# Performance work log

Measured on AMD Instinct MI355X. Metric: run time of the kernel, lower is better.

The kernel has to match this reference:

```python
import jax, jax.numpy as jnp
from jax import lax
import numpy as np

N = 262144    # input_size (mesh nodes)
B = 16        # batch of snapshots
LAT = 16      # dims_latent
HID = 512     # intermediate fc width
NFC = 16      # num_final_channels
START = 4097  # inv_conv_start
SPLIT = NFC * START
SFC = 2       # number of space-filling curves
K, S, P = 32, 4, 16             # kernel/stride/padding (dimension==2)
OPS = (1, 1, 0)                 # output_paddings of decoder convT chain
CH = ((16, 8), (8, 4), (4, 1))  # (in,out) channels per decoder convT layer


def conv_t(x, w, b, op):
    # torch ConvTranspose1d: w [Cin,Cout,K], stride=S, padding=P, output_padding=op
    # equivalent to lhs-dilated cross-correlation with flipped, transposed kernel
    rhs = jnp.flip(w, -1).transpose(1, 0, 2)  # [Cout,Cin,K]
    y = lax.conv_general_dilated(x, rhs, (1,), [(K - 1 - P, K - 1 - P + op)],
                                 lhs_dilation=(S,),
                                 dimension_numbers=('NCH', 'OIH', 'NCH'))
    return y + b[None, :, None]


def setup_inputs() -> dict:
    key = jax.random.key(0)
    ks = jax.random.split(key, 32)
    inp = {}
    inp['x'] = jax.random.normal(ks[0], (B, LAT), jnp.float32)
    inp['fc1_w'] = jax.random.normal(ks[1], (LAT, HID), jnp.float32) * 0.1
    inp['fc1_b'] = jnp.zeros((HID,), jnp.float32)
    inp['fc2_w'] = jax.random.normal(ks[2], (HID, SFC * SPLIT), jnp.float32) * 0.02
    inp['fc2_b'] = jnp.zeros((SFC * SPLIT,), jnp.float32)
    idx = 3
    for i in range(SFC):
        for j, (ci, co) in enumerate(CH):
            inp[f'ct{i}{j}_w'] = jax.random.normal(ks[idx], (ci, co, K), jnp.float32) * 0.05
            inp[f'ct{i}{j}_b'] = jnp.zeros((co,), jnp.float32)
            idx += 1
        # NearestNeighbouring(size=N, initial_weight=1/3, num_neigh=3)
        inp[f'sp{i}_w'] = jnp.full((N, 3), 1.0 / 3.0, jnp.float32)
        inp[f'sp{i}_b'] = jnp.zeros((N,), jnp.float32)
        oi = jax.random.permutation(ks[idx], N).astype(jnp.int32)
        idx += 1
        inp[f'ord{i}'] = oi
        inp[f'minus{i}'] = jnp.concatenate([oi[:1], oi[:-1]])  # find_minus_neigh
        inp[f'plus{i}'] = jnp.concatenate([oi[1:], oi[-1:]])   # find_plus_neigh
    # final_sp: NearestNeighbouring(size=N, initial_weight=1/sfc_nums, num_neigh=sfc_nums)
    inp['fsp_w'] = jnp.full((N, SFC), 1.0 / SFC, jnp.float32)
    inp['fsp_b'] = jnp.zeros((N,), jnp.float32)
    return inp


def reference(x, fc1_w, fc1_b, fc2_w, fc2_b,
              ct00_w, ct00_b, ct01_w, ct01_b, ct02_w, ct02_b,
              ct10_w, ct10_b, ct11_w, ct11_b, ct12_w, ct12_b,
              sp0_w, sp0_b, sp1_w, sp1_b, fsp_w, fsp_b,
              ord0, minus0, plus0, ord1, minus1, plus1):
    act = jnp.tanh  # unstructured default activation
    h = act(x @ fc1_w + fc1_b)
    h = act(h @ fc2_w + fc2_b)          # [B, SFC*SPLIT]
    h = h.reshape(-1, SPLIT, SFC)
    cts = (((ct00_w, ct00_b), (ct01_w, ct01_b), (ct02_w, ct02_b)),
           ((ct10_w, ct10_b), (ct11_w, ct11_b), (ct12_w, ct12_b)))
    sps = ((sp0_w, sp0_b), (sp1_w, sp1_b))
    ords = ((minus0, ord0, plus0), (minus1, ord1, plus1))
    zs = []
    for i in range(SFC):
        b = h[..., i].reshape(-1, NFC, START)   # [B,16,4097]
        for j in range(len(CH)):
            w, bb = cts[i][j]
            b = act(conv_t(b, w, bb, OPS[j]))
        b = b.reshape(-1, N)                    # [B, N]
        m, o, p = ords[i]
        # SFC gather of (minus, self, plus) neighbors -> [B, N, 3]
        tt = jnp.stack([b[:, m], b[:, o], b[:, p]], axis=-1)
        w, bb = sps[i]
        zs.append(act(jnp.sum(tt * w, -1) + bb))
    # combine the SFC branches with the final learned weighted sum
    z = act(jnp.sum(jnp.stack(zs, -1) * fsp_w, -1) + fsp_b)  # [B, N]
    return z
```

## Files before the change

### kernel.cpp

```cpp
#include <hip/hip_runtime.h>
#include <hip/hip_bf16.h>

#define BATCH 16
#define LAT 16
#define HID 512
#define NFC 16
#define START_ 4097
#define NSFC 2
#define NMESH 262144
#define JTOT 131104
#define HB_BR_STRIDE 1048832

#define L1 16385
#define L1S 16388
#define L2 65537
#define L2S 65540
#define L3 262144

#define Y1_SZ (BATCH*8*L1S)
#define Y2_SZ (BATCH*4*L2S)
#define Y3_SZ (BATCH*L3)

__global__ __launch_bounds__(256) void k_fc1(const float* __restrict__ x,
                                             const float* __restrict__ w,
                                             const float* __restrict__ bias,
                                             float* __restrict__ h1) {
    int j = blockIdx.x * 256 + threadIdx.x;
    float acc[BATCH];
    float bv = bias[j];
#pragma unroll
    for (int b = 0; b < BATCH; ++b) acc[b] = bv;
#pragma unroll
    for (int k = 0; k < LAT; ++k) {
        float wv = w[k * HID + j];
#pragma unroll
        for (int b = 0; b < BATCH; ++b)
            acc[b] = fmaf(x[b * LAT + k], wv, acc[b]);
    }
#pragma unroll
    for (int b = 0; b < BATCH; ++b) h1[b * HID + j] = tanhf(acc[b]);
}

__global__ __launch_bounds__(256) void k_fc2(const float* __restrict__ h1,
                                             const float* __restrict__ w,
                                             const float* __restrict__ bias,
                                             float* __restrict__ hb) {
    int j = blockIdx.x * 256 + threadIdx.x;
    if (j >= JTOT) return;
    float acc[BATCH];
    float bv = bias[j];
#pragma unroll
    for (int b = 0; b < BATCH; ++b) acc[b] = bv;
#pragma unroll 8
    for (int k = 0; k < HID; ++k) {
        float wv = w[(size_t)k * JTOT + j];
#pragma unroll
        for (int b = 0; b < BATCH; ++b)
            acc[b] = fmaf(h1[b * HID + k], wv, acc[b]);
    }
    int i = j & 1;
    int s = j >> 1;
    int c = s / START_;
    int t = s - c * START_;
    float* hp = hb + (size_t)i * HB_BR_STRIDE + c * START_ + t;
#pragma unroll
    for (int b = 0; b < BATCH; ++b)
        hp[(size_t)b * (NFC * START_)] = tanhf(acc[b]);
}

template <int CIN, int COUT, int WCO, int WT>
__global__ __launch_bounds__(256) void k_conv(const float* __restrict__ xb,
                                              float* __restrict__ yb,
                                              const float* __restrict__ w0g,
                                              const float* __restrict__ w1g,
                                              const float* __restrict__ b0g,
                                              const float* __restrict__ b1g,
                                              int LIN, int LINS, int LOUT, int LOUTS,
                                              int xbs, int ybs) {
    constexpr int SROW = WT * 256 + 12;
    constexpr int SROW4 = SROW / 4;
    __shared__ __align__(16) float sx[CIN * SROW];

    const int br = blockIdx.z;
    const float* x = xb + (size_t)br * xbs;
    float* y = yb + (size_t)br * ybs;
    const float* wg = br ? w1g : w0g;
    const float* bg = br ? b1g : b0g;
    const int b = blockIdx.y;
    const int t0 = blockIdx.x * (WT * 1024);
    const int q0 = (t0 + 16) >> 2;

    for (int idx = threadIdx.x; idx < CIN * SROW; idx += 256) {
        int ci = idx / SROW;
        int sr = idx - ci * SROW;
        int s = q0 - 8 + sr;
        sx[idx] = (s >= 0 && s < LIN) ? x[(size_t)(b * CIN + ci) * LINS + s] : 0.f;
    }
    __syncthreads();

    const int wv = __builtin_amdgcn_readfirstlane((int)(threadIdx.x >> 6));
    const int lane = threadIdx.x & 63;
    constexpr int WAVES_CO = 4 / WT;
    const int wt = wv / WAVES_CO;
    const int co0 = (wv % WAVES_CO) * WCO;

    float acc[WCO][16];
#pragma unroll
    for (int cw = 0; cw < WCO; ++cw) {
        float bv = bg[co0 + cw];
#pragma unroll
        for (int e = 0; e < 16; ++e) acc[cw][e] = bv;
    }

    const int qrel4 = wt * 64 + lane;
    const float4* sx4 = (const float4*)sx;
#pragma unroll 1
    for (int ci = 0; ci < CIN; ++ci) {
        float4 A = sx4[ci * SROW4 + qrel4];
        float4 Bv = sx4[ci * SROW4 + qrel4 + 1];
        float4 Cv = sx4[ci * SROW4 + qrel4 + 2];
        float xv[12] = {A.x, A.y, A.z, A.w, Bv.x, Bv.y, Bv.z, Bv.w,
                        Cv.x, Cv.y, Cv.z, Cv.w};
        const float* wp = wg + (ci * COUT + co0) * 32;
#pragma unroll
        for (int cw = 0; cw < WCO; ++cw) {
            const float* wpc = wp + cw * 32;
#pragma unroll
            for (int d = 0; d < 8; ++d)
#pragma unroll
                for (int m = 0; m < 4; ++m)
#pragma unroll
                    for (int j = 0; j < 4; ++j)
                        acc[cw][m * 4 + j] =
                            fmaf(xv[m + 8 - d], wpc[4 * d + j], acc[cw][m * 4 + j]);
        }
    }

    const int t_lane = t0 + wt * 1024 + lane * 16;
#pragma unroll
    for (int cw = 0; cw < WCO; ++cw) {
        float* yp = y + (size_t)(b * COUT + co0 + cw) * LOUTS + t_lane;
        if (t_lane + 15 < LOUT) {
#pragma unroll
            for (int c4 = 0; c4 < 4; ++c4) {
                float4 o;
                o.x = tanhf(acc[cw][c4 * 4 + 0]);
                o.y = tanhf(acc[cw][c4 * 4 + 1]);
                o.z = tanhf(acc[cw][c4 * 4 + 2]);
                o.w = tanhf(acc[cw][c4 * 4 + 3]);
                ((float4*)yp)[c4] = o;
            }
        } else {
            for (int e = 0; e < 16; ++e)
                if (t_lane + e < LOUT) yp[e] = tanhf(acc[cw][e]);
        }
    }
}

__global__ __launch_bounds__(256) void k_final(const float* __restrict__ y30,
                                               const float* __restrict__ y31,
                                               const int* __restrict__ ord0,
                                               const int* __restrict__ ord1,
                                               const float* __restrict__ sw0,
                                               const float* __restrict__ sb0,
                                               const float* __restrict__ sw1,
                                               const float* __restrict__ sb1,
                                               const float* __restrict__ fw,
                                               const float* __restrict__ fb,
                                               float* __restrict__ out) {
    __shared__ int i0[258], i1[258];
    __shared__ float c0[258], c1[258];
    const int tid = threadIdx.x;
    const int n0 = blockIdx.x * 256;
    const int n = n0 + tid;

    for (int jj = tid; jj < 258; jj += 256) {
        int nn = n0 - 1 + jj;
        nn = nn < 0 ? 0 : (nn > NMESH - 1 ? NMESH - 1 : nn);
        i0[jj] = ord0[nn];
        i1[jj] = ord1[nn];
    }

    const float w00 = sw0[n * 3], w01 = sw0[n * 3 + 1], w02 = sw0[n * 3 + 2];
    const float w10 = sw1[n * 3], w11 = sw1[n * 3 + 1], w12 = sw1[n * 3 + 2];
    const float s0b = sb0[n], s1b = sb1[n];
    const float f0 = fw[n * 2], f1 = fw[n * 2 + 1], fbv = fb[n];

    for (int b = 0; b < BATCH; ++b) {
        __syncthreads();
        for (int jj = tid; jj < 258; jj += 256) {
            c0[jj] = y30[b * NMESH + i0[jj]];
            c1[jj] = y31[b * NMESH + i1[jj]];
        }
        __syncthreads();
        float z0 = tanhf(w00 * c0[tid] + w01 * c0[tid + 1] + w02 * c0[tid + 2] + s0b);
        float z1 = tanhf(w10 * c1[tid] + w11 * c1[tid + 1] + w12 * c1[tid + 2] + s1b);
        out[b * NMESH + n] = tanhf(f0 * z0 + f1 * z1 + fbv);
    }
}

extern "C" void kernel_launch(void* const* d_in, const int* in_sizes, int n_in,
                              void* d_out, int out_size, void* d_ws, size_t ws_size,
                              hipStream_t stream) {
    const float* x     = (const float*)d_in[0];
    const float* fc1_w = (const float*)d_in[1];
    const float* fc1_b = (const float*)d_in[2];
    const float* fc2_w = (const float*)d_in[3];
    const float* fc2_b = (const float*)d_in[4];
    const float* ctw[2][3] = {{(const float*)d_in[5], (const float*)d_in[7], (const float*)d_in[9]},
                              {(const float*)d_in[16], (const float*)d_in[18], (const float*)d_in[20]}};
    const float* ctb[2][3] = {{(const float*)d_in[6], (const float*)d_in[8], (const float*)d_in[10]},
                              {(const float*)d_in[17], (const float*)d_in[19], (const float*)d_in[21]}};
    const float* sp0w = (const float*)d_in[11];
    const float* sp0b = (const float*)d_in[12];
    const int*   ord0 = (const int*)d_in[13];
    const float* sp1w = (const float*)d_in[22];
    const float* sp1b = (const float*)d_in[23];
    const int*   ord1 = (const int*)d_in[24];
    const float* fspw = (const float*)d_in[27];
    const float* fspb = (const float*)d_in[28];
    float* out = (float*)d_out;
    float* ws = (float*)d_ws;

    const size_t OFF_H1 = 0;
    const size_t OFF_HB = 8192;
    const size_t OFF_Y1p = OFF_HB + 2ull * HB_BR_STRIDE;
    const size_t OFF_Y2p = OFF_Y1p + 2ull * Y1_SZ;
    const size_t OFF_Y3p = OFF_Y2p + 2ull * Y2_SZ;
    const size_t END_P = OFF_Y3p + 2ull * Y3_SZ;
    const size_t OFF_Y1s = OFF_HB + 2ull * HB_BR_STRIDE;
    const size_t OFF_Y2s = OFF_Y1s + (size_t)Y1_SZ;
    const size_t OFF_Y3s = OFF_Y2s + (size_t)Y2_SZ;

    const bool par = ws_size >= END_P * sizeof(float);

    k_fc1<<<2, 256, 0, stream>>>(x, fc1_w, fc1_b, ws + OFF_H1);
    k_fc2<<<(JTOT + 255) / 256, 256, 0, stream>>>(ws + OFF_H1, fc2_w, fc2_b, ws + OFF_HB);

    float* y3_0;
    float* y3_1;
    if (par) {
        float* hb = ws + OFF_HB;
        float* y1 = ws + OFF_Y1p;
        float* y2 = ws + OFF_Y2p;
        float* y3 = ws + OFF_Y3p;
        k_conv<16, 8, 2, 1><<<dim3(17, BATCH, 2), 256, 0, stream>>>(
            hb, y1, ctw[0][0], ctw[1][0], ctb[0][0], ctb[1][0],
            START_, START_, L1, L1S, HB_BR_STRIDE, Y1_SZ);
        k_conv<8, 4, 1, 1><<<dim3(65, BATCH, 2), 256, 0, stream>>>(
            y1, y2, ctw[0][1], ctw[1][1], ctb[0][1], ctb[1][1],
            L1, L1S, L2, L2S, Y1_SZ, Y2_SZ);
        k_conv<4, 1, 1, 4><<<dim3(64, BATCH, 2), 256, 0, stream>>>(
            y2, y3, ctw[0][2], ctw[1][2], ctb[0][2], ctb[1][2],
            L2, L2S, L3, L3, Y2_SZ, Y3_SZ);
        y3_0 = y3;
        y3_1 = y3 + Y3_SZ;
    } else {
        float* y1 = ws + OFF_Y1s;
        float* y2 = ws + OFF_Y2s;
        for (int i = 0; i < 2; ++i) {
            float* hb_i = ws + OFF_HB + (size_t)i * HB_BR_STRIDE;
            float* y3_i = ws + OFF_Y3s + (size_t)i * Y3_SZ;
            k_conv<16, 8, 2, 1><<<dim3(17, BATCH, 1), 256, 0, stream>>>(
                hb_i, y1, ctw[i][0], ctw[i][0], ctb[i][0], ctb[i][0],
                START_, START_, L1, L1S, 0, 0);
            k_conv<8, 4, 1, 1><<<dim3(65, BATCH, 1), 256, 0, stream>>>(
                y1, y2, ctw[i][1], ctw[i][1], ctb[i][1], ctb[i][1],
                L1, L1S, L2, L2S, 0, 0);
            k_conv<4, 1, 1, 4><<<dim3(64, BATCH, 1), 256, 0, stream>>>(
                y2, y3_i, ctw[i][2], ctw[i][2], ctb[i][2], ctb[i][2],
                L2, L2S, L3, L3, 0, 0);
        }
        y3_0 = ws + OFF_Y3s;
        y3_1 = ws + OFF_Y3s + Y3_SZ;
    }

    k_final<<<NMESH / 256, 256, 0, stream>>>(y3_0, y3_1, ord0, ord1,
                                             sp0w, sp0b, sp1w, sp1b,
                                             fspw, fspb, out);
}
```

Measured before the change: 602.2 us.

## Write last convT output node-major so final gather loads contiguous batch vectors

Adds a dedicated kernel for the final transposed convolution that handles all 16 batches per thread and writes its output transposed as [node][batch]. The final SFC gather kernel then fetches each permuted neighbour's 16 batch values with float4 loads instead of 16 separate scattered scalar loads, and it synchronises once rather than twice per batch. The aim is to replace the random-access gather traffic, which wastes most of each fetched cache line, with contiguous 64-byte reads. The cost is more registers in the conv kernel (64 accumulators), a new launch geometry of 256 blocks per branch, and larger shared-memory buffers in the final kernel.

```diff
diff --git a/kernel.cpp b/kernel.cpp
--- a/kernel.cpp
+++ b/kernel.cpp
@@ -157,8 +157,78 @@
     }
 }
 
-__global__ __launch_bounds__(256) void k_final(const float* __restrict__ y30,
-                                               const float* __restrict__ y31,
+#define C3_TT 1024
+#define C3_SW 264
+
+__global__ __launch_bounds__(256) void k_conv3t(const float* __restrict__ y2g,
+                                                float* __restrict__ y3t,
+                                                const float* __restrict__ w0g,
+                                                const float* __restrict__ w1g,
+                                                const float* __restrict__ b0g,
+                                                const float* __restrict__ b1g,
+                                                int xbs, int ybs) {
+    __shared__ __align__(16) float sx[BATCH * 4 * C3_SW];
+
+    const int br = blockIdx.z;
+    const float* x = y2g + (size_t)br * xbs;
+    float* y = y3t + (size_t)br * ybs;
+    const float* wg = br ? w1g : w0g;
+    const float bv = (br ? b1g : b0g)[0];
+
+    const int t0 = blockIdx.x * C3_TT;
+    const int q0 = (t0 >> 2) + 4;
+    const int s0 = q0 - 7;
+
+    for (int idx = threadIdx.x; idx < BATCH * 4 * C3_SW; idx += 256) {
+        int row = idx / C3_SW;
+        int col = idx - row * C3_SW;
+        int s = s0 + col;
+        sx[idx] = (col < 263 && s >= 0 && s < L2) ? x[(size_t)row * L2S + s] : 0.f;
+    }
+    __syncthreads();
+
+    const int tq = threadIdx.x;
+    float acc[4][BATCH];
+#pragma unroll
+    for (int r = 0; r < 4; ++r)
+#pragma unroll
+        for (int b = 0; b < BATCH; ++b) acc[r][b] = bv;
+
+#pragma unroll
+    for (int ci = 0; ci < 4; ++ci) {
+        const float* wp = wg + ci * 32;
+#pragma unroll
+        for (int b = 0; b < BATCH; ++b) {
+            const float* sp = sx + (b * 4 + ci) * C3_SW + tq;
+            float xv[8];
+#pragma unroll
+            for (int j = 0; j < 8; ++j) xv[j] = sp[j];
+#pragma unroll
+            for (int d = 0; d < 8; ++d)
+#pragma unroll
+                for (int r = 0; r < 4; ++r)
+                    acc[r][b] = fmaf(xv[7 - d], wp[4 * d + r], acc[r][b]);
+        }
+    }
+
+    const int tbase = t0 + 4 * tq;
+#pragma unroll
+    for (int r = 0; r < 4; ++r) {
+        float* yp = y + (size_t)(tbase + r) * BATCH;
+#pragma unroll
+        for (int v = 0; v < 4; ++v) {
+            float4 o;
+            o.x = tanhf(acc[r][4 * v + 0]);
+            o.y = tanhf(acc[r][4 * v + 1]);
+            o.z = tanhf(acc[r][4 * v + 2]);
+            o.w = tanhf(acc[r][4 * v + 3]);
+            ((float4*)yp)[v] = o;
+        }
+    }
+}
+
+__global__ __launch_bounds__(256) void k_final(const float* __restrict__ y3t0,
+                                               const float* __restrict__ y3t1,
                                                const int* __restrict__ ord0,
                                                const int* __restrict__ ord1,
                                                const float* __restrict__ sw0,
@@ -169,7 +239,7 @@
                                                const float* __restrict__ fb,
                                                float* __restrict__ out) {
     __shared__ int i0[258], i1[258];
-    __shared__ float c0[258], c1[258];
+    __shared__ float c0[BATCH][264], c1[BATCH][264];
     const int tid = threadIdx.x;
     const int n0 = blockIdx.x * 256;
     const int n = n0 + tid;
@@ -180,21 +250,33 @@
         i0[jj] = ord0[nn];
         i1[jj] = ord1[nn];
     }
+    __syncthreads();
+
+    for (int kk = tid; kk < 258 * 4; kk += 256) {
+        int jj = kk >> 2;
+        int v = kk & 3;
+        float4 a = *(const float4*)(y3t0 + (size_t)i0[jj] * BATCH + v * 4);
+        c0[v * 4 + 0][jj] = a.x;
+        c0[v * 4 + 1][jj] = a.y;
+        c0[v * 4 + 2][jj] = a.z;
+        c0[v * 4 + 3][jj] = a.w;
+        float4 bq = *(const float4*)(y3t1 + (size_t)i1[jj] * BATCH + v * 4);
+        c1[v * 4 + 0][jj] = bq.x;
+        c1[v * 4 + 1][jj] = bq.y;
+        c1[v * 4 + 2][jj] = bq.z;
+        c1[v * 4 + 3][jj] = bq.w;
+    }
 
     const float w00 = sw0[n * 3], w01 = sw0[n * 3 + 1], w02 = sw0[n * 3 + 2];
     const float w10 = sw1[n * 3], w11 = sw1[n * 3 + 1], w12 = sw1[n * 3 + 2];
     const float s0b = sb0[n], s1b = sb1[n];
     const float f0 = fw[n * 2], f1 = fw[n * 2 + 1], fbv = fb[n];
-
+    __syncthreads();
+
+#pragma unroll
     for (int b = 0; b < BATCH; ++b) {
-        __syncthreads();
-        for (int jj = tid; jj < 258; jj += 256) {
-            c0[jj] = y30[b * NMESH + i0[jj]];
-            c1[jj] = y31[b * NMESH + i1[jj]];
-        }
-        __syncthreads();
-        float z0 = tanhf(w00 * c0[tid] + w01 * c0[tid + 1] + w02 * c0[tid + 2] + s0b);
-        float z1 = tanhf(w10 * c1[tid] + w11 * c1[tid + 1] + w12 * c1[tid + 2] + s1b);
+        float z0 = tanhf(w00 * c0[b][tid] + w01 * c0[b][tid + 1] + w02 * c0[b][tid + 2] + s0b);
+        float z1 = tanhf(w10 * c1[b][tid] + w11 * c1[b][tid + 1] + w12 * c1[b][tid + 2] + s1b);
         out[b * NMESH + n] = tanhf(f0 * z0 + f1 * z1 + fbv);
     }
 }
@@ -250,9 +332,9 @@
         k_conv<8, 4, 1, 1><<<dim3(65, BATCH, 2), 256, 0, stream>>>(
             y1, y2, ctw[0][1], ctw[1][1], ctb[0][1], ctb[1][1],
             L1, L1S, L2, L2S, Y1_SZ, Y2_SZ);
-        k_conv<4, 1, 1, 4><<<dim3(64, BATCH, 2), 256, 0, stream>>>(
+        k_conv3t<<<dim3(L3 / C3_TT, 1, 2), 256, 0, stream>>>(
             y2, y3, ctw[0][2], ctw[1][2], ctb[0][2], ctb[1][2],
-            L2, L2S, L3, L3, Y2_SZ, Y3_SZ);
+            Y2_SZ, Y3_SZ);
         y3_0 = y3;
         y3_1 = y3 + Y3_SZ;
     } else {
@@ -267,9 +349,9 @@
             k_conv<8, 4, 1, 1><<<dim3(65, BATCH, 1), 256, 0, stream>>>(
                 y1, y2, ctw[i][1], ctw[i][1], ctb[i][1], ctb[i][1],
                 L1, L1S, L2, L2S, 0, 0);
-            k_conv<4, 1, 1, 4><<<dim3(64, BATCH, 1), 256, 0, stream>>>(
+            k_conv3t<<<dim3(L3 / C3_TT, 1, 1), 256, 0, stream>>>(
                 y2, y3_i, ctw[i][2], ctw[i][2], ctb[i][2], ctb[i][2],
-                L2, L2S, L3, L3, 0, 0);
+                0, 0);
         }
         y3_0 = ws + OFF_Y3s;
         y3_1 = ws + OFF_Y3s + Y3_SZ;
```

Measured after the change: 868.6 us. 44.2% more time.
